# Kernel tuning notes

Measured on AMD Instinct MI355X. Metric: run time of the kernel, lower is better.

The kernel has to match this reference:

```python
import jax, jax.numpy as jnp
import numpy as np

B, M, D, H = 2, 2048, 1024, 16
DH = D // H            # 64 head dim
R_ATTN = 512           # rank of q/k/v SVD factors
FFN_D = 2048           # GEGLU inner dim; Wi out = 2*FFN_D
R_FFN = 1024           # rank of FFN SVD factors
ROPE_BASE = 10000.0
LN_EPS = 1e-5


def _layernorm(x, g, b):
    mu = jnp.mean(x, axis=-1, keepdims=True)
    var = jnp.mean(jnp.square(x - mu), axis=-1, keepdims=True)
    return (x - mu) * jax.lax.rsqrt(var + LN_EPS) * g + b


def _rotate_half(x):
    x1, x2 = jnp.split(x, 2, axis=-1)
    return jnp.concatenate((-x2, x1), axis=-1)


def _rope_cos_sin(m, dh, dtype):
    inv_freq = 1.0 / (ROPE_BASE ** (jnp.arange(0, dh, 2, dtype=jnp.float32) / dh))
    freqs = jnp.arange(m, dtype=jnp.float32)[:, None] * inv_freq[None, :]  # [M, dh/2]
    emb = jnp.concatenate((freqs, freqs), axis=-1)  # [M, dh]
    return jnp.cos(emb).astype(dtype), jnp.sin(emb).astype(dtype)


def setup_inputs() -> dict:
    key = jax.random.key(0)
    ks = iter(jax.random.split(key, 32))
    rn = lambda shape, s: jax.random.normal(next(ks), shape, jnp.float32) * s
    w = 0.02
    return {
        'hidden_states': rn((B, M, D), 1.0),
        'ln1_g': jnp.ones((D,), jnp.float32), 'ln1_b': jnp.zeros((D,), jnp.float32),
        'Uq': rn((D, R_ATTN), w), 'Vq': rn((R_ATTN, D), w), 'bq': rn((D,), w),
        'Uk': rn((D, R_ATTN), w), 'Vk': rn((R_ATTN, D), w), 'bk': rn((D,), w),
        'Uv': rn((D, R_ATTN), w), 'Vv': rn((R_ATTN, D), w), 'bv': rn((D,), w),
        'Wo': rn((D, D), w), 'bo': rn((D,), w),  # dense attn out proj, torch [out,in]
        'ln2_g': jnp.ones((D,), jnp.float32), 'ln2_b': jnp.zeros((D,), jnp.float32),
        'U1': rn((D, R_FFN), w), 'V1': rn((R_FFN, 2 * FFN_D), w), 'b1': rn((2 * FFN_D,), w),
        'U2': rn((FFN_D, R_FFN), w), 'V2': rn((R_FFN, D), w), 'b2': rn((D,), w),
    }


def reference(hidden_states, ln1_g, ln1_b, Uq, Vq, bq, Uk, Vk, bk, Uv, Vv, bv,
              Wo, bo, ln2_g, ln2_b, U1, V1, b1, U2, V2, b2):
    x = hidden_states
    xn = _layernorm(x, ln1_g, ln1_b)
    # low-rank QKV: y = (x @ U) @ V + b
    q = (xn @ Uq) @ Vq + bq
    k = (xn @ Uk) @ Vk + bk
    v = (xn @ Uv) @ Vv + bv
    to_bhmd = lambda t: t.reshape(B, M, H, DH).transpose(0, 2, 1, 3)
    q, k, v = to_bhmd(q), to_bhmd(k), to_bhmd(v)
    cos, sin = _rope_cos_sin(M, DH, q.dtype)  # [M, DH]
    q = q * cos + _rotate_half(q) * sin
    k = k * cos + _rotate_half(k) * sin
    scale = 1.0 / np.sqrt(DH)
    scores = jnp.einsum('bhmd,bhnd->bhmn', q, k) * scale  # [B,H,M,M]
    attn = jax.nn.softmax(scores, axis=-1)
    out = jnp.einsum('bhmn,bhnd->bhmd', attn, v)
    out = out.transpose(0, 2, 1, 3).reshape(B, M, D)
    x = x + out @ Wo.T + bo
    # low-rank GEGLU FFN
    xn2 = _layernorm(x, ln2_g, ln2_b)
    z = (xn2 @ U1) @ V1 + b1  # [B,M,2*FFN_D]
    z1, z2 = jnp.split(z, 2, axis=-1)
    h = jax.nn.gelu(z1, approximate=True) * z2  # GEGLU, tanh approx
    y = (h @ U2) @ V2 + b2
    return x + y
```

## Files before the change

### kernel.cpp

```cpp
#include <hip/hip_runtime.h>


typedef unsigned short u16;
typedef unsigned int u32;
typedef u16 u16x8 __attribute__((ext_vector_type(8)));
typedef __bf16 bf16x8 __attribute__((ext_vector_type(8)));
typedef float f32x4 __attribute__((ext_vector_type(4)));

__device__ __forceinline__ u16 f2bf(float f) {
    u32 u = __builtin_bit_cast(u32, f);
    u += 0x7fff + ((u >> 16) & 1);
    return (u16)(u >> 16);
}
__device__ __forceinline__ float bf2f(u16 h) {
    u32 u = ((u32)h) << 16;
    return __builtin_bit_cast(float, u);
}
__device__ __forceinline__ u32 packbf(float a, float b) {
    return __builtin_amdgcn_perm(__builtin_bit_cast(u32, b),
                                 __builtin_bit_cast(u32, a), 0x07060302u);
}

__device__ __forceinline__ void gload16(const void* g, void* l) {
    __builtin_amdgcn_global_load_lds(
        (const __attribute__((address_space(1))) void*)g,
        (__attribute__((address_space(3))) void*)l, 16, 0, 0);
}

#define MB 1048576u
#define OFF_UQKVT (0*MB)
#define OFF_VQKVT (3*MB)
#define OFF_WOB   (6*MB)
#define OFF_U1T   (8*MB)
#define OFF_V1TP  (10*MB)
#define OFF_U2T   (18*MB)
#define OFF_V2T   (22*MB)
#define OFF_BQKV  (24*MB)
#define OFF_B1P   (24*MB + 16384u)
#define OFF_XN    (25*MB)
#define OFF_TBUF  (33*MB)
#define OFF_QB    (45*MB)
#define OFF_KB    (53*MB)
#define OFF_HB    (45*MB)
#define OFF_VTB   (61*MB)
#define OFF_OB    (69*MB)
#define OFF_X2    (93*MB)

__global__ __launch_bounds__(256) void prep_kernel(
    const float* __restrict__ Uq, const float* __restrict__ Uk,
    const float* __restrict__ Uv, const float* __restrict__ Vq,
    const float* __restrict__ Vk, const float* __restrict__ Vv,
    const float* __restrict__ Wo, const float* __restrict__ U1,
    const float* __restrict__ V1, const float* __restrict__ U2,
    const float* __restrict__ V2,
    const float* __restrict__ bq, const float* __restrict__ bk,
    const float* __restrict__ bv, const float* __restrict__ b1,
    u16* __restrict__ UQKVT, u16* __restrict__ VQKVT, u16* __restrict__ WOB,
    u16* __restrict__ U1T, u16* __restrict__ V1TP, u16* __restrict__ U2T,
    u16* __restrict__ V2T, float* __restrict__ BQKV, float* __restrict__ B1P)
{
    __shared__ float tile[32][33];
    int bid = blockIdx.x;

    if (bid >= 12288) {
        int id = (bid - 12288) * 256 + threadIdx.x;
        if (id < 3072) {
            float v = (id < 1024) ? bq[id] : (id < 2048 ? bk[id - 1024] : bv[id - 2048]);
            BQKV[id] = v;
        }
        int g = id >> 7, q = id & 127;
        B1P[id] = b1[(q < 64) ? (g*64 + q) : (2048 + g*64 + (q - 64))];
        return;
    }
    if (bid >= 11264) {
        int i4 = ((bid - 11264) * 256 + threadIdx.x) * 4;
        float4 v = *(const float4*)(Wo + i4);
        u16 tmp[4] = {f2bf(v.x), f2bf(v.y), f2bf(v.z), f2bf(v.w)};
        *(uint2*)(WOB + i4) = *(const uint2*)tmp;
        return;
    }

    const float* src; u16* dst; int K, N, src_ld, nx; bool gg = false;
    if (bid < 3072) {
        int t = bid / 512; bid -= t * 512;
        if (t < 3) { src = t==0 ? Uq : (t==1 ? Uk : Uv);
                     dst = UQKVT + t * 512*1024; K = 1024; N = 512; src_ld = 512; nx = 16; }
        else { int z = t - 3; src = z==0 ? Vq : (z==1 ? Vk : Vv);
               dst = VQKVT + z * 524288; K = 512; N = 1024; src_ld = 1024; nx = 32; }
    } else if (bid < 4096)  { src = U1; dst = U1T;  K = 1024; N = 1024; src_ld = 1024; nx = 32;  bid -= 3072; }
    else if (bid < 8192)    { src = V1; dst = V1TP; K = 1024; N = 4096; src_ld = 4096; nx = 128; bid -= 4096; gg = true; }
    else if (bid < 10240)   { src = U2; dst = U2T;  K = 2048; N = 1024; src_ld = 1024; nx = 32;  bid -= 8192; }
    else                    { src = V2; dst = V2T;  K = 1024; N = 1024; src_ld = 1024; nx = 32;  bid -= 10240; }

    int tx = threadIdx.x & 31, ty = threadIdx.x >> 5;
    int n0 = (bid % nx) * 32, k0 = (bid / nx) * 32;
    int srccol;
    if (gg) { int p = n0 + tx; int g = p >> 7, q = p & 127;
              srccol = (q < 64) ? (g*64 + q) : (2048 + g*64 + (q - 64)); }
    else srccol = n0 + tx;
    for (int i = 0; i < 4; i++)
        tile[ty + i*8][tx] = src[(size_t)(k0 + ty + i*8) * src_ld + srccol];
    __syncthreads();
    for (int i = 0; i < 4; i++)
        dst[(size_t)(n0 + ty + i*8) * K + k0 + tx] = f2bf(tile[tx][ty + i*8]);
}

__global__ __launch_bounds__(256) void ln_kernel(
    const float* __restrict__ x, const float* __restrict__ g,
    const float* __restrict__ bta, u16* __restrict__ out)
{
    int w = threadIdx.x >> 6, lane = threadIdx.x & 63;
    int row = blockIdx.x * 4 + w;
    const float* xr = x + (size_t)row * 1024;
    float vals[16];
    float s = 0.f, s2 = 0.f;
    #pragma unroll
    for (int ii = 0; ii < 16; ii++) {
        float v = xr[lane + ii*64];
        vals[ii] = v; s += v; s2 += v * v;
    }
    #pragma unroll
    for (int off = 1; off < 64; off <<= 1) {
        s  += __shfl_xor(s, off);
        s2 += __shfl_xor(s2, off);
    }
    float mu = s * (1.f/1024.f);
    float var = s2 * (1.f/1024.f) - mu * mu;
    float rs = rsqrtf(var + 1e-5f);
    #pragma unroll
    for (int ii = 0; ii < 16; ii++) {
        int col = lane + ii*64;
        out[(size_t)row * 1024 + col] = f2bf((vals[ii] - mu) * rs * g[col] + bta[col]);
    }
}

template<int V>
__global__ __launch_bounds__(512, 2) void gemm256_geglu_kernel(
    const u16* __restrict__ A, const u16* __restrict__ Bt,
    u16* __restrict__ hb, const float* __restrict__ bias, int Kdim)
{
    constexpr bool S = (V==0 || V==2 || V==3);
    constexpr bool D = (V==0 || V==1 || V==2);
    constexpr bool E = (V==0 || V==1 || V==3);

    __shared__ u16 As[2][16384];
    __shared__ u16 Bs[2][16384];
    int tid = threadIdx.x;
    int wg = (blockIdx.x & 7) * 32 + (blockIdx.x >> 3);
    int m0 = (wg >> 4) * 256, n0 = (wg & 15) * 256;
    int w = tid >> 6, lane = tid & 63, quad = lane >> 4, l15 = lane & 15;
    int wr = (w >> 2) * 16, wc = (w & 3) * 16;
    int xsw = l15 & 7;
    int s0 = (quad ^ xsw) * 8, s1 = s0 ^ 32;

    int srow = tid >> 3;
    int scol = ((tid & 7) ^ (srow & 7)) * 8;
    const u16* Ap = A  + (size_t)(m0 + srow) * Kdim + scol;
    const u16* Bp = Bt + (size_t)(n0 + srow) * Kdim + scol;

    int abase = (wr + l15) * 64;
    int bbase = (wc + l15) * 64;

    f32x4 acc[8][4] = {};

#define STG_A(buf, t, h) do {                                                      \
    gload16(Ap + (size_t)(t)*64 + (size_t)((h)*128     )*Kdim,                     \
            &As[buf][(h)*8192 + tid*8]);                                           \
    gload16(Ap + (size_t)(t)*64 + (size_t)((h)*128 + 64)*Kdim,                     \
            &As[buf][(h)*8192 + 4096 + tid*8]);                                    \
} while (0)
#define STG_B(buf, t, h) do {                                                      \
    gload16(Bp + (size_t)(t)*64 + (size_t)((h)*128     )*Kdim,                     \
            &Bs[buf][(h)*8192 + tid*8]);                                           \
    gload16(Bp + (size_t)(t)*64 + (size_t)((h)*128 + 64)*Kdim,                     \
            &Bs[buf][(h)*8192 + 4096 + tid*8]);                                    \
} while (0)
#define SB()  __builtin_amdgcn_sched_barrier(0)

    int nt = Kdim >> 6;

    STG_A(0, 0, 0); STG_A(0, 0, 1); STG_B(0, 0, 0); STG_B(0, 0, 1);
    STG_A(1, 1, 0); STG_A(1, 1, 1); STG_B(1, 1, 0); STG_B(1, 1, 1);
    asm volatile("s_waitcnt vmcnt(8)" ::: "memory");
    __builtin_amdgcn_s_barrier();
    SB();

    bf16x8 afl[4][2], afh[4][2], bfl[2][2], bfh[2][2];
    {
        const u16* A0 = As[0];
        const u16* B0 = Bs[0];
        #pragma unroll
        for (int i = 0; i < 4; i++) {
            afl[i][0] = *(const bf16x8*)&A0[abase + i*2048 + s0];
            afl[i][1] = *(const bf16x8*)&A0[abase + i*2048 + s1];
        }
        #pragma unroll
        for (int j = 0; j < 2; j++) {
            bfl[j][0] = *(const bf16x8*)&B0[bbase + j*4096 + s0];
            bfl[j][1] = *(const bf16x8*)&B0[bbase + j*4096 + s1];
        }
    }
    if constexpr (!D) {
        #pragma unroll
        for (int i = 0; i < 4; i++) { afh[i][0] = afl[i][0]; afh[i][1] = afl[i][1]; }
        #pragma unroll
        for (int j = 0; j < 2; j++) { bfh[j][0] = bfl[j][0]; bfh[j][1] = bfl[j][1]; }
    }

    for (int t = 0; t < nt; ++t) {
        int buf = t & 1;
        const u16* Asc = As[buf];
        const u16* Bsc = Bs[buf];
        const u16* Asn = As[buf ^ 1];
        const u16* Bsn = Bs[buf ^ 1];
        bool more = (t + 1 < nt);
        bool st   = (t + 2 < nt);

        if constexpr (D) {
            #pragma unroll
            for (int j = 0; j < 2; j++) {
                bfh[j][0] = *(const bf16x8*)&Bsc[bbase + 8192 + j*4096 + s0];
                bfh[j][1] = *(const bf16x8*)&Bsc[bbase + 8192 + j*4096 + s1];
            }
            SB();
        }
        __builtin_amdgcn_s_setprio(1);
        #pragma unroll
        for (int i = 0; i < 4; i++)
            #pragma unroll
            for (int j = 0; j < 2; j++) {
                acc[i][j] = __builtin_amdgcn_mfma_f32_16x16x32_bf16(afl[i][0], bfl[j][0], acc[i][j], 0, 0, 0);
                acc[i][j] = __builtin_amdgcn_mfma_f32_16x16x32_bf16(afl[i][1], bfl[j][1], acc[i][j], 0, 0, 0);
            }
        __builtin_amdgcn_s_setprio(0);

        if constexpr (D) {
            #pragma unroll
            for (int i = 0; i < 4; i++) {
                afh[i][0] = *(const bf16x8*)&Asc[abase + 8192 + i*2048 + s0];
                afh[i][1] = *(const bf16x8*)&Asc[abase + 8192 + i*2048 + s1];
            }
            SB();
        }
        __builtin_amdgcn_s_setprio(1);
        #pragma unroll
        for (int i = 0; i < 4; i++)
            #pragma unroll
            for (int j = 0; j < 2; j++) {
                acc[i][2+j] = __builtin_amdgcn_mfma_f32_16x16x32_bf16(afl[i][0], bfh[j][0], acc[i][2+j], 0, 0, 0);
                acc[i][2+j] = __builtin_amdgcn_mfma_f32_16x16x32_bf16(afl[i][1], bfh[j][1], acc[i][2+j], 0, 0, 0);
            }
        __builtin_amdgcn_s_setprio(0);

        if (more) {
            SB();
            asm volatile("s_waitcnt lgkmcnt(0)" ::: "memory");
            __builtin_amdgcn_s_barrier();
            SB();
            if constexpr (S) {
                if (st) { STG_A(buf, t+2, 0); STG_A(buf, t+2, 1);
                          STG_B(buf, t+2, 0); STG_B(buf, t+2, 1); }
                SB();
                if (st) asm volatile("s_waitcnt vmcnt(8)" ::: "memory");
                else    asm volatile("s_waitcnt vmcnt(0)" ::: "memory");
            }
            __builtin_amdgcn_s_barrier();
            SB();
            if constexpr (D) {
                #pragma unroll
                for (int i = 0; i < 4; i++) {
                    afl[i][0] = *(const bf16x8*)&Asn[abase + i*2048 + s0];
                    afl[i][1] = *(const bf16x8*)&Asn[abase + i*2048 + s1];
                }
                SB();
            }
        }

        __builtin_amdgcn_s_setprio(1);
        #pragma unroll
        for (int i = 0; i < 4; i++)
            #pragma unroll
            for (int j = 0; j < 2; j++) {
                acc[4+i][j] = __builtin_amdgcn_mfma_f32_16x16x32_bf16(afh[i][0], bfl[j][0], acc[4+i][j], 0, 0, 0);
                acc[4+i][j] = __builtin_amdgcn_mfma_f32_16x16x32_bf16(afh[i][1], bfl[j][1], acc[4+i][j], 0, 0, 0);
            }
        __builtin_amdgcn_s_setprio(0);

        if constexpr (D) {
            if (more) {
                #pragma unroll
                for (int j = 0; j < 2; j++) {
                    bfl[j][0] = *(const bf16x8*)&Bsn[bbase + j*4096 + s0];
                    bfl[j][1] = *(const bf16x8*)&Bsn[bbase + j*4096 + s1];
                }
                SB();
            }
        }
        __builtin_amdgcn_s_setprio(1);
        #pragma unroll
        for (int i = 0; i < 4; i++)
            #pragma unroll
            for (int j = 0; j < 2; j++) {
                acc[4+i][2+j] = __builtin_amdgcn_mfma_f32_16x16x32_bf16(afh[i][0], bfh[j][0], acc[4+i][2+j], 0, 0, 0);
                acc[4+i][2+j] = __builtin_amdgcn_mfma_f32_16x16x32_bf16(afh[i][1], bfh[j][1], acc[4+i][2+j], 0, 0, 0);
            }
        __builtin_amdgcn_s_setprio(0);
    }
#undef STG_A
#undef STG_B
#undef SB

    if constexpr (E) {
        #pragma unroll
        for (int mi = 0; mi < 8; mi++) {
            int row = m0 + wr + mi*32 + quad*4;
            #pragma unroll
            for (int p = 0; p < 2; p++) {
                int c1 = n0 + p*128 + wc + l15;
                float bz1 = bias[c1], bz2 = bias[c1 + 64];
                int hcol = (n0 >> 1) + p*64 + wc + l15;
                #pragma unroll
                for (int r = 0; r < 4; r++) {
                    float z1 = acc[mi][2*p][r] + bz1;
                    float z2 = acc[mi][2*p+1][r] + bz2;
                    float uu = 0.7978845608028654f * (z1 + 0.044715f * z1 * z1 * z1);
                    float e = __expf(2.f * uu);
                    float th = (e - 1.f) / (e + 1.f);
                    float hv = 0.5f * z1 * (1.f + th) * z2;
                    hb[(size_t)(row + r) * 2048 + hcol] = f2bf(hv);
                }
            }
        }
    } else {
        f32x4 ssum = {};
        #pragma unroll
        for (int mi = 0; mi < 8; mi++)
            #pragma unroll
            for (int j = 0; j < 4; j++)
                ssum += acc[mi][j];
        ((f32x4*)hb)[(size_t)blockIdx.x * 512 + tid] = ssum;
    }
}

__global__ __launch_bounds__(256) void gemm_bt64_kernel(
    const u16* __restrict__ A, int lda, const u16* __restrict__ Bt,
    void* __restrict__ Cout, int ldc, const float* __restrict__ bias,
    const float* __restrict__ resid, int Kdim, int mode)
{
    __shared__ u16 As[2][4096];
    __shared__ u16 Bs[2][2048];
    int tid = threadIdx.x;
    int m0 = blockIdx.y * 128, n0 = blockIdx.x * 64;
    int w = tid >> 6, lane = tid & 63, quad = lane >> 4, l15 = lane & 15;
    int wm = (w >> 1) * 64, wn = (w & 1) * 32;
    int sr = tid >> 2, sc8 = (tid & 3) * 8;

    f32x4 acc[4][2] = {};

    const u16* Ap = A  + (size_t)(m0 + sr) * lda  + sc8;
    const u16* Bp = Bt + (size_t)(n0 + sr) * Kdim + sc8;

    #define GSTAGE64(buf, koff) do {                                       \
        gload16(Ap + (koff),                     &As[buf][tid * 8]);       \
        gload16(Ap + (koff) + (size_t)64 * lda,  &As[buf][2048 + tid*8]);  \
        gload16(Bp + (koff),                     &Bs[buf][tid * 8]);       \
    } while (0)

    GSTAGE64(0, 0);
    __syncthreads();

    for (int k0 = 0; k0 < Kdim; k0 += 32) {
        int cur = (k0 >> 5) & 1;
        if (k0 + 32 < Kdim) GSTAGE64(cur ^ 1, k0 + 32);
        const u16* Asc = As[cur];
        const u16* Bsc = Bs[cur];
        bf16x8 af[4], bfr[2];
        #pragma unroll
        for (int i = 0; i < 4; i++)
            af[i] = *(const bf16x8*)&Asc[(wm + i*16 + l15) * 32 + quad * 8];
        #pragma unroll
        for (int j = 0; j < 2; j++)
            bfr[j] = *(const bf16x8*)&Bsc[(wn + j*16 + l15) * 32 + quad * 8];
        #pragma unroll
        for (int i = 0; i < 4; i++)
            #pragma unroll
            for (int j = 0; j < 2; j++)
                acc[i][j] = __builtin_amdgcn_mfma_f32_16x16x32_bf16(af[i], bfr[j], acc[i][j], 0, 0, 0);
        __syncthreads();
    }
    #undef GSTAGE64

    #pragma unroll
    for (int i = 0; i < 4; i++) {
        int row = m0 + wm + i*16 + quad*4;
        #pragma unroll
        for (int j = 0; j < 2; j++) {
            int col = n0 + wn + j*16 + l15;
            float bv = bias ? bias[col] : 0.f;
            #pragma unroll
            for (int r = 0; r < 4; r++) {
                float v = acc[i][j][r] + bv;
                size_t idx = (size_t)(row + r) * ldc + col;
                if (mode == 0) ((float*)Cout)[idx] = v + resid[idx];
                else           ((u16*)Cout)[idx] = f2bf(v);
            }
        }
    }
}

__global__ __launch_bounds__(256) void qkv2_kernel(
    const u16* __restrict__ T, const u16* __restrict__ Vw,
    const float* __restrict__ bqkv, u16* __restrict__ qout,
    u16* __restrict__ kout, u16* __restrict__ vtout)
{
    __shared__ u16 As[2][4096];
    __shared__ u16 Bs[2][4096];
    int tid = threadIdx.x;
    int z = blockIdx.z;
    int m0 = blockIdx.y * 128, n0 = blockIdx.x * 128;
    int w = tid >> 6, lane = tid & 63, quad = lane >> 4, l15 = lane & 15;
    int wm = (w >> 1) * 64, wn = (w & 1) * 64;
    int sr = tid >> 2, sc8 = (tid & 3) * 8;

    f32x4 acc[4][4] = {};

    const u16* Ap = T  + (size_t)z * 512 + (size_t)(m0 + sr) * 1536 + sc8;
    const u16* Bp = Vw + (size_t)z * 512 * 1024 + (size_t)(n0 + sr) * 512 + sc8;

    #define QSTAGE(buf, koff) do {                                        \
        gload16(Ap + (koff),                     &As[buf][tid * 8]);      \
        gload16(Ap + (koff) + (size_t)64 * 1536, &As[buf][2048 + tid*8]); \
        gload16(Bp + (koff),                     &Bs[buf][tid * 8]);      \
        gload16(Bp + (koff) + (size_t)64 * 512,  &Bs[buf][2048 + tid*8]); \
    } while (0)

    QSTAGE(0, 0);
    __syncthreads();

    for (int k0 = 0; k0 < 512; k0 += 32) {
        int cur = (k0 >> 5) & 1;
        if (k0 + 32 < 512) QSTAGE(cur ^ 1, k0 + 32);
        const u16* Asc = As[cur];
        const u16* Bsc = Bs[cur];
        bf16x8 af[4], bfr[4];
        #pragma unroll
        for (int i = 0; i < 4; i++)
            af[i] = *(const bf16x8*)&Asc[(wm + i*16 + l15) * 32 + quad * 8];
        #pragma unroll
        for (int j = 0; j < 4; j++)
            bfr[j] = *(const bf16x8*)&Bsc[(wn + j*16 + l15) * 32 + quad * 8];
        #pragma unroll
        for (int i = 0; i < 4; i++)
            #pragma unroll
            for (int j = 0; j < 4; j++)
                acc[i][j] = __builtin_amdgcn_mfma_f32_16x16x32_bf16(af[i], bfr[j], acc[i][j], 0, 0, 0);
        __syncthreads();
    }
    #undef QSTAGE

    const float* bias = bqkv + z * 1024;
    if (z < 2) {
        u16* Ob = z ? kout : qout;
        float qscale = z ? 1.f : 0.18033688011112042f;
        #pragma unroll
        for (int i = 0; i < 4; i++) {
            int row0 = m0 + wm + i*16 + quad*4;
            #pragma unroll
            for (int j = 0; j < 2; j++) {
                int col = n0 + wn + j*16 + l15;
                float bj = bias[col], bj2 = bias[col + 32];
                float invf = exp2f((float)(col & 31) * -0.4152410118609203f);
                #pragma unroll
                for (int r = 0; r < 4; r++) {
                    int t = row0 + r;
                    float fr = (float)(t & 2047) * invf;
                    float sn, cs;
                    __sincosf(fr, &sn, &cs);
                    sn *= qscale; cs *= qscale;
                    float v1 = acc[i][j][r] + bj;
                    float v2 = acc[i][j+2][r] + bj2;
                    Ob[(size_t)t * 1024 + col]      = f2bf(v1 * cs - v2 * sn);
                    Ob[(size_t)t * 1024 + col + 32] = f2bf(v2 * cs + v1 * sn);
                }
            }
        }
    } else {
        int bb = m0 >> 11;
        #pragma unroll
        for (int i = 0; i < 4; i++) {
            int row0 = m0 + wm + i*16 + quad*4;
            #pragma unroll
            for (int j = 0; j < 4; j++) {
                int col = n0 + wn + j*16 + l15;
                float bj = bias[col];
                u16 pack[4];
                #pragma unroll
                for (int r = 0; r < 4; r++) pack[r] = f2bf(acc[i][j][r] + bj);
                size_t dst = ((size_t)(bb * 16 + (col >> 6)) * 64 + (col & 63)) * 2048 + (row0 & 2047);
                *(uint2*)&vtout[dst] = *(const uint2*)pack;
            }
        }
    }
}

__global__ __launch_bounds__(256) void attn_kernel(
    const u16* __restrict__ Q, const u16* __restrict__ K,
    const u16* __restrict__ Vt, u16* __restrict__ O)
{
    __shared__ u16 Ps[128 * 72];
    int tid = threadIdx.x;
    int bh = blockIdx.x;
    int b = bh >> 4, h = bh & 15;
    int m0 = blockIdx.y * 128;
    int w = tid >> 6, lane = tid & 63, quad = lane >> 4, l15 = lane & 15;
    int wm = w * 32;
    size_t qkbase = (size_t)b * 2048 * 1024 + h * 64;
    const u16* Kg = K + qkbase;
    const u16* Vg = Vt + (size_t)bh * 64 * 2048;

    bf16x8 qf[2][2];
    #pragma unroll
    for (int i = 0; i < 2; i++)
        #pragma unroll
        for (int ks = 0; ks < 2; ks++)
            qf[i][ks] = *(const bf16x8*)(Q + qkbase +
                (size_t)(m0 + wm + i*16 + l15) * 1024 + ks*32 + quad*8);

    f32x4 oacc[2][4] = {};
    float lsum[2] = {};

    for (int kt = 0; kt < 32; kt++) {
        int key0 = kt * 64;

        f32x4 sacc[4][2] = {};
        #pragma unroll
        for (int ks = 0; ks < 2; ks++) {
            bf16x8 kf[4];
            #pragma unroll
            for (int jj = 0; jj < 4; jj++)
                kf[jj] = *(const bf16x8*)(Kg +
                    (size_t)(key0 + jj*16 + l15) * 1024 + ks*32 + quad*8);
            #pragma unroll
            for (int jj = 0; jj < 4; jj++)
                #pragma unroll
                for (int i = 0; i < 2; i++)
                    sacc[jj][i] = __builtin_amdgcn_mfma_f32_16x16x32_bf16(kf[jj], qf[i][ks], sacc[jj][i], 0, 0, 0);
        }

        #pragma unroll
        for (int i = 0; i < 2; i++) {
            int prow = (wm + i*16 + l15) * 72 + quad*4;
            #pragma unroll
            for (int jj = 0; jj < 4; jj++) {
                float p0 = __builtin_amdgcn_exp2f(sacc[jj][i][0]);
                float p1 = __builtin_amdgcn_exp2f(sacc[jj][i][1]);
                float p2 = __builtin_amdgcn_exp2f(sacc[jj][i][2]);
                float p3 = __builtin_amdgcn_exp2f(sacc[jj][i][3]);
                lsum[i] += (p0 + p1) + (p2 + p3);
                uint2 pk; pk.x = packbf(p0, p1); pk.y = packbf(p2, p3);
                *(uint2*)&Ps[prow + jj*16] = pk;
            }
        }

        #pragma unroll
        for (int ks = 0; ks < 2; ks++) {
            bf16x8 pf[2], vf[4];
            #pragma unroll
            for (int i = 0; i < 2; i++)
                pf[i] = *(const bf16x8*)&Ps[(wm + i*16 + l15) * 72 + ks*32 + quad*8];
            #pragma unroll
            for (int j = 0; j < 4; j++)
                vf[j] = *(const bf16x8*)(Vg +
                    (size_t)(j*16 + l15) * 2048 + key0 + ks*32 + quad*8);
            #pragma unroll
            for (int i = 0; i < 2; i++)
                #pragma unroll
                for (int j = 0; j < 4; j++)
                    oacc[i][j] = __builtin_amdgcn_mfma_f32_16x16x32_bf16(pf[i], vf[j], oacc[i][j], 0, 0, 0);
        }
    }

    float inv[2][4];
    #pragma unroll
    for (int i = 0; i < 2; i++) {
        float s = lsum[i];
        s += __shfl_xor(s, 16);
        s += __shfl_xor(s, 32);
        #pragma unroll
        for (int r = 0; r < 4; r++)
            inv[i][r] = 1.f / __shfl(s, (lane & 48) | (quad*4 + r));
    }
    #pragma unroll
    for (int i = 0; i < 2; i++)
        #pragma unroll
        for (int r = 0; r < 4; r++) {
            int row = m0 + wm + i*16 + quad*4 + r;
            #pragma unroll
            for (int j = 0; j < 4; j++)
                O[qkbase + (size_t)row * 1024 + j*16 + l15] = f2bf(oacc[i][j][r] * inv[i][r]);
        }
}

extern "C" void kernel_launch(void* const* d_in, const int* in_sizes, int n_in,
                              void* d_out, int out_size, void* d_ws, size_t ws_size,
                              hipStream_t stream) {
    (void)n_in; (void)out_size; (void)ws_size;
    const float* x     = (const float*)d_in[0];
    const float* ln1_g = (const float*)d_in[1];
    const float* ln1_b = (const float*)d_in[2];
    const float* Uq    = (const float*)d_in[3];
    const float* Vq    = (const float*)d_in[4];
    const float* bq    = (const float*)d_in[5];
    const float* Uk    = (const float*)d_in[6];
    const float* Vk    = (const float*)d_in[7];
    const float* bk    = (const float*)d_in[8];
    const float* Uv    = (const float*)d_in[9];
    const float* Vv    = (const float*)d_in[10];
    const float* bv    = (const float*)d_in[11];
    const float* Wo    = (const float*)d_in[12];
    const float* bo    = (const float*)d_in[13];
    const float* ln2_g = (const float*)d_in[14];
    const float* ln2_b = (const float*)d_in[15];
    const float* U1    = (const float*)d_in[16];
    const float* V1    = (const float*)d_in[17];
    const float* b1    = (const float*)d_in[18];
    const float* U2    = (const float*)d_in[19];
    const float* V2    = (const float*)d_in[20];
    const float* b2    = (const float*)d_in[21];
    float* out = (float*)d_out;
    char* ws = (char*)d_ws;

    u16* UQKVT = (u16*)(ws + OFF_UQKVT);
    u16* VQKVT = (u16*)(ws + OFF_VQKVT);
    u16* WOB   = (u16*)(ws + OFF_WOB);
    u16* U1T   = (u16*)(ws + OFF_U1T);
    u16* V1TP  = (u16*)(ws + OFF_V1TP);
    u16* U2T   = (u16*)(ws + OFF_U2T);
    u16* V2T   = (u16*)(ws + OFF_V2T);
    float* BQKV = (float*)(ws + OFF_BQKV);
    float* B1P  = (float*)(ws + OFF_B1P);
    u16* xn  = (u16*)(ws + OFF_XN);
    u16* tbuf= (u16*)(ws + OFF_TBUF);
    u16* qb  = (u16*)(ws + OFF_QB);
    u16* kb  = (u16*)(ws + OFF_KB);
    u16* vtb = (u16*)(ws + OFF_VTB);
    u16* ob  = (u16*)(ws + OFF_OB);
    u16* hb  = (u16*)(ws + OFF_HB);
    u16* scr = (u16*)(ws + OFF_VTB);
    float* x2 = (float*)(ws + OFF_X2);

    prep_kernel<<<12304, 256, 0, stream>>>(
        Uq, Uk, Uv, Vq, Vk, Vv, Wo, U1, V1, U2, V2, bq, bk, bv, b1,
        UQKVT, VQKVT, WOB, U1T, V1TP, U2T, V2T, BQKV, B1P);

    ln_kernel<<<1024, 256, 0, stream>>>(x, ln1_g, ln1_b, xn);

    gemm_bt64_kernel<<<dim3(24, 32), 256, 0, stream>>>(xn, 1024, UQKVT, tbuf, 1536,
                                                       nullptr, nullptr, 1024, 1);
    qkv2_kernel<<<dim3(8, 32, 3), 256, 0, stream>>>(tbuf, VQKVT, BQKV, qb, kb, vtb);

    attn_kernel<<<dim3(32, 16), 256, 0, stream>>>(qb, kb, vtb, ob);

    gemm_bt64_kernel<<<dim3(16, 32), 256, 0, stream>>>(ob, 1024, WOB, x2, 1024,
                                                       bo, x, 1024, 0);
    ln_kernel<<<1024, 256, 0, stream>>>(x2, ln2_g, ln2_b, xn);

    gemm_bt64_kernel<<<dim3(16, 32), 256, 0, stream>>>(xn, 1024, U1T, tbuf, 1024,
                                                       nullptr, nullptr, 1024, 1);
    gemm256_geglu_kernel<0><<<dim3(256), 512, 0, stream>>>(tbuf, V1TP, hb, B1P, 1024);
    if (in_sizes[0] < 0) {
        gemm256_geglu_kernel<1><<<dim3(256), 512, 0, stream>>>(tbuf, V1TP, scr, B1P, 1024);
        gemm256_geglu_kernel<2><<<dim3(256), 512, 0, stream>>>(tbuf, V1TP, scr, B1P, 1024);
        gemm256_geglu_kernel<3><<<dim3(256), 512, 0, stream>>>(tbuf, V1TP, scr, B1P, 1024);
        gemm256_geglu_kernel<4><<<dim3(256), 512, 0, stream>>>(tbuf, V1TP, scr, B1P, 1024);
    }
    gemm_bt64_kernel<<<dim3(16, 32), 256, 0, stream>>>(hb, 2048, U2T, tbuf, 1024,
                                                       nullptr, nullptr, 2048, 1);
    gemm_bt64_kernel<<<dim3(16, 32), 256, 0, stream>>>(tbuf, 1024, V2T, out, 1024,
                                                       b2, x2, 1024, 0);
}
```

Before: 476.2 us.

## Stage K/V tiles through double-buffered swizzled LDS in attention kernel

```diff
diff --git a/kernel.cpp b/kernel.cpp
--- a/kernel.cpp
+++ b/kernel.cpp
@@ -503,11 +503,14 @@
     }
 }
 
+#define PSTR 88
 __global__ __launch_bounds__(256) void attn_kernel(
     const u16* __restrict__ Q, const u16* __restrict__ K,
     const u16* __restrict__ Vt, u16* __restrict__ O)
 {
-    __shared__ u16 Ps[128 * 72];
+    __shared__ u16 Ks[2][64 * 64];
+    __shared__ u16 Vs[2][64 * 64];
+    __shared__ u16 Ps[128 * PSTR];
     int tid = threadIdx.x;
     int bh = blockIdx.x;
     int b = bh >> 4, h = bh & 15;
@@ -515,7 +518,6 @@
     int w = tid >> 6, lane = tid & 63, quad = lane >> 4, l15 = lane & 15;
     int wm = w * 32;
     size_t qkbase = (size_t)b * 2048 * 1024 + h * 64;
-    const u16* Kg = K + qkbase;
     const u16* Vg = Vt + (size_t)bh * 64 * 2048;
 
     bf16x8 qf[2][2];
@@ -529,56 +531,95 @@
     f32x4 oacc[2][4] = {};
     float lsum[2] = {};
 
-    for (int kt = 0; kt < 32; kt++) {
-        int key0 = kt * 64;
-
-        f32x4 sacc[4][2] = {};
-        #pragma unroll
-        for (int ks = 0; ks < 2; ks++) {
-            bf16x8 kf[4];
-            #pragma unroll
-            for (int jj = 0; jj < 4; jj++)
-                kf[jj] = *(const bf16x8*)(Kg +
-                    (size_t)(key0 + jj*16 + l15) * 1024 + ks*32 + quad*8);
-            #pragma unroll
-            for (int jj = 0; jj < 4; jj++)
-                #pragma unroll
-                for (int i = 0; i < 2; i++)
-                    sacc[jj][i] = __builtin_amdgcn_mfma_f32_16x16x32_bf16(kf[jj], qf[i][ks], sacc[jj][i], 0, 0, 0);
-        }
-
-        #pragma unroll
-        for (int i = 0; i < 2; i++) {
-            int prow = (wm + i*16 + l15) * 72 + quad*4;
-            #pragma unroll
-            for (int jj = 0; jj < 4; jj++) {
-                float p0 = __builtin_amdgcn_exp2f(sacc[jj][i][0]);
-                float p1 = __builtin_amdgcn_exp2f(sacc[jj][i][1]);
-                float p2 = __builtin_amdgcn_exp2f(sacc[jj][i][2]);
-                float p3 = __builtin_amdgcn_exp2f(sacc[jj][i][3]);
-                lsum[i] += (p0 + p1) + (p2 + p3);
-                uint2 pk; pk.x = packbf(p0, p1); pk.y = packbf(p2, p3);
-                *(uint2*)&Ps[prow + jj*16] = pk;
-            }
-        }
-
-        #pragma unroll
-        for (int ks = 0; ks < 2; ks++) {
-            bf16x8 pf[2], vf[4];
-            #pragma unroll
-            for (int i = 0; i < 2; i++)
-                pf[i] = *(const bf16x8*)&Ps[(wm + i*16 + l15) * 72 + ks*32 + quad*8];
-            #pragma unroll
-            for (int j = 0; j < 4; j++)
-                vf[j] = *(const bf16x8*)(Vg +
-                    (size_t)(j*16 + l15) * 2048 + key0 + ks*32 + quad*8);
-            #pragma unroll
-            for (int i = 0; i < 2; i++)
-                #pragma unroll
-                for (int j = 0; j < 4; j++)
-                    oacc[i][j] = __builtin_amdgcn_mfma_f32_16x16x32_bf16(pf[i], vf[j], oacc[i][j], 0, 0, 0);
-        }
-    }
+    int r0 = tid >> 3, p = tid & 7;
+    int c0 = (p ^ (r0 & 7)) * 8;
+    int xsw = l15 & 7;
+
+    const u16* kp = K + qkbase + (size_t)r0 * 1024 + c0;
+    const u16* vp = Vg + (size_t)r0 * 2048 + c0;
+
+    #define STG(bufl) do {                                                      \
+        gload16(kp,             &Ks[bufl][r0 * 64 + p * 8]);                    \
+        gload16(kp + 32*1024,   &Ks[bufl][(r0 + 32) * 64 + p * 8]);             \
+        gload16(vp,             &Vs[bufl][r0 * 64 + p * 8]);                    \
+        gload16(vp + 32*2048,   &Vs[bufl][(r0 + 32) * 64 + p * 8]);             \
+        kp += 64*1024; vp += 64;                                                \
+    } while (0)
+
+    #define SYNC() do {                                                         \
+        asm volatile("s_waitcnt lgkmcnt(0)" ::: "memory");                      \
+        asm volatile("s_waitcnt vmcnt(0)" ::: "memory");                        \
+        __builtin_amdgcn_s_barrier();                                           \
+    } while (0)
+
+    #define BODY(bufl) do {                                                     \
+        f32x4 sacc[4][2] = {};                                                  \
+        _Pragma("unroll")                                                       \
+        for (int ks = 0; ks < 2; ks++) {                                        \
+            bf16x8 kf[4];                                                       \
+            _Pragma("unroll")                                                   \
+            for (int jj = 0; jj < 4; jj++)                                      \
+                kf[jj] = *(const bf16x8*)&Ks[bufl][(jj*16 + l15) * 64 +         \
+                                                   (((ks*4 + quad) ^ xsw) * 8)];\
+            _Pragma("unroll")                                                   \
+            for (int jj = 0; jj < 4; jj++)                                      \
+                _Pragma("unroll")                                               \
+                for (int i = 0; i < 2; i++)                                     \
+                    sacc[jj][i] = __builtin_amdgcn_mfma_f32_16x16x32_bf16(      \
+                        kf[jj], qf[i][ks], sacc[jj][i], 0, 0, 0);               \
+        }                                                                       \
+        _Pragma("unroll")                                                       \
+        for (int i = 0; i < 2; i++) {                                           \
+            int prow = (wm + i*16 + l15) * PSTR + quad*4;                       \
+            _Pragma("unroll")                                                   \
+            for (int jj = 0; jj < 4; jj++) {                                    \
+                float p0 = __builtin_amdgcn_exp2f(sacc[jj][i][0]);              \
+                float p1 = __builtin_amdgcn_exp2f(sacc[jj][i][1]);              \
+                float p2 = __builtin_amdgcn_exp2f(sacc[jj][i][2]);              \
+                float p3 = __builtin_amdgcn_exp2f(sacc[jj][i][3]);              \
+                lsum[i] += (p0 + p1) + (p2 + p3);                               \
+                uint2 pk; pk.x = packbf(p0, p1); pk.y = packbf(p2, p3);         \
+                *(uint2*)&Ps[prow + jj*16] = pk;                                \
+            }                                                                   \
+        }                                                                       \
+        _Pragma("unroll")                                                       \
+        for (int ks = 0; ks < 2; ks++) {                                        \
+            bf16x8 pf[2], vf[4];                                                \
+            _Pragma("unroll")                                                   \
+            for (int i = 0; i < 2; i++)                                         \
+                pf[i] = *(const bf16x8*)&Ps[(wm + i*16 + l15) * PSTR +          \
+                                            ks*32 + quad*8];                    \
+            _Pragma("unroll")                                                   \
+            for (int j = 0; j < 4; j++)                                         \
+                vf[j] = *(const bf16x8*)&Vs[bufl][(j*16 + l15) * 64 +           \
+                                                  (((ks*4 + quad) ^ xsw) * 8)]; \
+            _Pragma("unroll")                                                   \
+            for (int i = 0; i < 2; i++)                                         \
+                _Pragma("unroll")                                               \
+                for (int j = 0; j < 4; j++)                                     \
+                    oacc[i][j] = __builtin_amdgcn_mfma_f32_16x16x32_bf16(       \
+                        pf[i], vf[j], oacc[i][j], 0, 0, 0);                     \
+        }                                                                       \
+    } while (0)
+
+    STG(0);
+    SYNC();
+
+    for (int kt2 = 0; kt2 < 16; ++kt2) {
+        STG(1);
+        BODY(0);
+        SYNC();
+        if (kt2 < 15) {
+            STG(0);
+            BODY(1);
+            SYNC();
+        } else {
+            BODY(1);
+        }
+    }
+    #undef STG
+    #undef SYNC
+    #undef BODY
 
     float inv[2][4];
     #pragma unroll
```

After: 409.3 us. -14.1%, faster.
